# Optimization experiments

Measured on AMD Instinct MI355X. Metric: run time of the kernel, lower is better.

## Reference

```python
import jax, jax.numpy as jnp
import numpy as np

B, L, C, D, H, NB, K = 8, 1024, 4, 64, 8, 2, 16  # batch, seq, conds, dim, heads, blocks, rbf centers

def _ln(x, s, b):
    m = x.mean(-1, keepdims=True)
    v = x.var(-1, keepdims=True)
    return (x - m) / jnp.sqrt(v + 1e-6) * s + b

def setup_inputs() -> dict:
    key = jax.random.key(0)
    ks = jax.random.split(key, 24)
    rn = lambda i, shape, sc=0.02: jax.random.normal(ks[i], shape, jnp.float32) * sc
    inp = {}
    inp['z'] = jax.random.normal(ks[0], (B, L), jnp.float32)
    inp['conditionals'] = jax.random.normal(ks[1], (C,), jnp.float32)
    inp['s'] = jnp.sort(jax.random.uniform(ks[2], (L,), jnp.float32))
    inp['embed'] = rn(3, (L, 2 * D - (C + 1)))  # positional id embedding table
    # input MLP([4D, D]) with gelu
    inp['Win1'] = rn(4, (2 * D, 4 * D)); inp['bin1'] = jnp.zeros((4 * D,), jnp.float32)
    inp['Win2'] = rn(5, (4 * D, D));     inp['bin2'] = jnp.zeros((D,), jnp.float32)
    # per-block (leading dim NB) transformer params
    inp['ln1_s'] = jnp.ones((NB, D), jnp.float32); inp['ln1_b'] = jnp.zeros((NB, D), jnp.float32)
    inp['ln2_s'] = jnp.ones((NB, D), jnp.float32); inp['ln2_b'] = jnp.zeros((NB, D), jnp.float32)
    inp['Wq'] = rn(6, (NB, D, 2 * D)); inp['bq'] = jnp.zeros((NB, 2 * D), jnp.float32)
    inp['Wk'] = rn(7, (NB, D, 2 * D)); inp['bk'] = jnp.zeros((NB, 2 * D), jnp.float32)
    inp['Wv'] = rn(8, (NB, D, 2 * D)); inp['bv'] = jnp.zeros((NB, 2 * D), jnp.float32)
    inp['Wo'] = rn(9, (NB, 2 * D, D)); inp['bo'] = jnp.zeros((NB, D), jnp.float32)
    # RBF-network attention bias: features exp(-(d-c)^2/(2w^2)) -> linear to H heads
    inp['rbf_c'] = jnp.tile(jnp.linspace(-1.0, 1.0, K, dtype=jnp.float32)[None], (NB, 1))
    inp['rbf_logw'] = jnp.full((NB, K), -1.0, jnp.float32)
    inp['rbf_w'] = rn(10, (NB, K, H), 0.1); inp['rbf_b'] = jnp.zeros((NB, H), jnp.float32)
    # FFN MLP([4D, D])
    inp['W1'] = rn(11, (NB, D, 4 * D)); inp['b1'] = jnp.zeros((NB, 4 * D), jnp.float32)
    inp['W2'] = rn(12, (NB, 4 * D, D)); inp['b2'] = jnp.zeros((NB, D), jnp.float32)
    # head MLP([4D, D, 1])
    inp['Wh1'] = rn(13, (D, 4 * D)); inp['bh1'] = jnp.zeros((4 * D,), jnp.float32)
    inp['Wh2'] = rn(14, (4 * D, D)); inp['bh2'] = jnp.zeros((D,), jnp.float32)
    inp['Wh3'] = rn(15, (D, 1));     inp['bh3'] = jnp.zeros((1,), jnp.float32)
    return inp

def reference(z, conditionals, s, embed, Win1, bin1, Win2, bin2,
              ln1_s, ln1_b, ln2_s, ln2_b, Wq, bq, Wk, bk, Wv, bv, Wo, bo,
              rbf_c, rbf_logw, rbf_w, rbf_b, W1, b1, W2, b2,
              Wh1, bh1, Wh2, bh2, Wh3, bh3):
    Bn, Ln = z.shape
    Cn = conditionals.shape[0]
    Hn = rbf_w.shape[-1]
    dh = Wq.shape[-1] // Hn
    scale = 1.0 / jnp.sqrt(jnp.float32(dh))
    # cond_as_feats: [z, broadcast conditionals] -> (B, L, C+1); prepend ids embedding -> (B, L, 2D)
    feats = jnp.concatenate([
        jnp.broadcast_to(embed[None], (Bn,) + embed.shape),
        z[..., None],
        jnp.broadcast_to(conditionals[None, None, :], (Bn, Ln, Cn)),
    ], axis=-1)
    x = jax.nn.gelu(feats @ Win1 + bin1) @ Win2 + bin2  # (B, L, D)
    dist = s[:, None] - s[None, :]  # (L, L) pairwise query-key coordinate diff (same per batch)
    for i in range(Wq.shape[0]):
        h = _ln(x, ln1_s[i], ln1_b[i])
        q = (h @ Wq[i] + bq[i]).reshape(Bn, Ln, Hn, dh)
        k = (h @ Wk[i] + bk[i]).reshape(Bn, Ln, Hn, dh)
        v = (h @ Wv[i] + bv[i]).reshape(Bn, Ln, Hn, dh)
        scores = jnp.einsum('bqhd,bkhd->bhqk', q, k) * scale
        # RBF-network bias on pairwise distances, per head
        phi = jnp.exp(-(dist[..., None] - rbf_c[i]) ** 2 / (2.0 * jnp.exp(rbf_logw[i]) ** 2))  # (L, L, K)
        bias = jnp.einsum('qkf,fh->hqk', phi, rbf_w[i]) + rbf_b[i][:, None, None]  # (H, L, L)
        a = jax.nn.softmax(scores + bias[None], axis=-1)
        o = jnp.einsum('bhqk,bkhd->bqhd', a, v).reshape(Bn, Ln, Hn * dh)
        x = x + o @ Wo[i] + bo[i]
        h2 = _ln(x, ln2_s[i], ln2_b[i])
        x = x + jax.nn.gelu(h2 @ W1[i] + b1[i]) @ W2[i] + b2[i]
    hh = jax.nn.gelu(x @ Wh1 + bh1)
    hh = jax.nn.gelu(hh @ Wh2 + bh2)
    return hh @ Wh3 + bh3  # f_hat: (B, L, 1)
```

## Files before the change

kernel.cpp:

```cpp
#include <hip/hip_runtime.h>
#include <hip/hip_bf16.h>

#define BB   8
#define LL   1024
#define DD   64
#define D2   128
#define D4   256
#define HH   8
#define DH   16

typedef __attribute__((ext_vector_type(8))) short short8;
typedef __attribute__((ext_vector_type(4))) float floatx4;

#define OFF_WIN1   0
#define OFF_WIN2   65536
#define OFF_LAY0   98304
#define LAY_STRIDE 131072
#define OFF_WQ     0
#define OFF_WK     16384
#define OFF_WV     32768
#define OFF_WO     49152
#define OFF_W1     65536
#define OFF_W2     98304
#define OFF_WH1    360448
#define OFF_WH2    393216

__device__ __forceinline__ float gelu_tanh(float u) {
  float t = tanhf(0.7978845608028654f * (u + 0.044715f * u * u * u));
  return 0.5f * u * (1.0f + t);
}

__device__ __forceinline__ float wave_reduce_sum(float v) {
#pragma unroll
  for (int m = 32; m >= 1; m >>= 1) v += __shfl_xor(v, m, 64);
  return v;
}

__device__ __forceinline__ unsigned short f2bf(float x) {
  unsigned u = __float_as_uint(x);
  u += 0x7fffu + ((u >> 16) & 1u);
  return (unsigned short)(u >> 16);
}

__device__ __forceinline__ float bf2f(unsigned short x) {
  return __uint_as_float(((unsigned)x) << 16);
}

__device__ __forceinline__ void split_bf(float v, unsigned short& hi,
                                         unsigned short& lo) {
  hi = f2bf(v);
  lo = f2bf(v - bf2f(hi));
}

template <int K, int KP>
__device__ __forceinline__ floatx4 mfma_tile(
    const unsigned short* Ah, const unsigned short* Al,
    const unsigned short* __restrict__ Bh, const unsigned short* __restrict__ Bl,
    int lq, int quad, floatx4 C) {
#pragma unroll
  for (int kk = 0; kk < K; kk += 32) {
    short8 ah = *(const short8*)(Ah + lq * KP + kk + quad * 8);
    short8 al = *(const short8*)(Al + lq * KP + kk + quad * 8);
    short8 bh = *(const short8*)(Bh + lq * K + kk + quad * 8);
    short8 bl = *(const short8*)(Bl + lq * K + kk + quad * 8);
    C = __builtin_amdgcn_mfma_f32_16x16x32_bf16(ah, bh, C, 0, 0, 0);
    C = __builtin_amdgcn_mfma_f32_16x16x32_bf16(al, bh, C, 0, 0, 0);
    C = __builtin_amdgcn_mfma_f32_16x16x32_bf16(ah, bl, C, 0, 0, 0);
  }
  return C;
}

struct PrepArgs {
  const float* src[16];
  int Kd[16], Nd[16], dst[16], elems[16];
};

__global__ __launch_bounds__(256) void k_prep(PrepArgs a,
                                              unsigned short* __restrict__ arena) {
  int mid = blockIdx.y;
  int e = blockIdx.x * 256 + threadIdx.x;
  int KN = a.elems[mid];
  if (e >= KN) return;
  int K = a.Kd[mid], N = a.Nd[mid];
  int n = e / K, k = e - n * K;
  float wv = a.src[mid][k * N + n];
  unsigned short hi, lo;
  split_bf(wv, hi, lo);
  arena[a.dst[mid] + e] = hi;
  arena[a.dst[mid] + KN + e] = lo;
}

__global__ __launch_bounds__(256) void k_bias(
    const float* __restrict__ s, const float* __restrict__ rbf_c,
    const float* __restrict__ rbf_logw, const float* __restrict__ rbf_w,
    const float* __restrict__ rbf_b, unsigned short* __restrict__ biasT) {
  int lay = blockIdx.y;
  int id = blockIdx.x * 256 + threadIdx.x;
  int q = id >> 10, k = id & 1023;
  float dd = s[q] - s[k];
  float acc[8];
#pragma unroll
  for (int h = 0; h < 8; ++h) acc[h] = rbf_b[lay * 8 + h];
#pragma unroll 1
  for (int f = 0; f < 16; ++f) {
    float c = rbf_c[lay * 16 + f];
    float inv2w2 = 0.5f * __expf(-2.0f * rbf_logw[lay * 16 + f]);
    float e = dd - c;
    float ph = __expf(-e * e * inv2w2);
#pragma unroll
    for (int h = 0; h < 8; ++h)
      acc[h] = fmaf(ph, rbf_w[lay * 128 + f * 8 + h], acc[h]);
  }
  unsigned short* bT = biasT + (size_t)lay * 8 * 1024 * 1024;
#pragma unroll
  for (int h = 0; h < 8; ++h)
    bT[(size_t)(h * 1024 + q) * 1024 + k] = f2bf(acc[h]);
}

__device__ __forceinline__ void qkv_tail(
    const float* xl, unsigned short* Sh, unsigned short* Sl,
    const unsigned short* __restrict__ arena, int lay,
    const float* __restrict__ ln_s, const float* __restrict__ ln_b,
    const float* __restrict__ bq, const float* __restrict__ bk,
    const float* __restrict__ bv, unsigned short* __restrict__ qo,
    unsigned short* __restrict__ ko, unsigned short* __restrict__ voT,
    int tok0, int t) {
  int w = t >> 6, lane = t & 63;
  int lq = lane & 15, quad = lane >> 4;
  float ss = ln_s[lay * 64 + lane], sb = ln_b[lay * 64 + lane];
#pragma unroll
  for (int tk = 0; tk < 4; ++tk) {
    int tok = w * 4 + tk;
    float v = xl[tok * 64 + lane];
    float mean = wave_reduce_sum(v) * 0.015625f;
    float d = v - mean;
    float var = wave_reduce_sum(d * d) * 0.015625f;
    float hv = d * rsqrtf(var + 1e-6f) * ss + sb;
    unsigned short hi, lo;
    split_bf(hv, hi, lo);
    Sh[tok * 72 + lane] = hi;
    Sl[tok * 72 + lane] = lo;
  }
  __syncthreads();
  int b = tok0 >> 10, l0 = tok0 & 1023;
#pragma unroll 1
  for (int mat = 0; mat < 3; ++mat) {
    const unsigned short* Bh =
        arena + OFF_LAY0 + lay * LAY_STRIDE + mat * 16384;
    const unsigned short* Bl = Bh + 8192;
    const float* bias = (mat == 0 ? bq : mat == 1 ? bk : bv) + lay * 128;
#pragma unroll
    for (int j = 0; j < 2; ++j) {
      int tl = w + j * 4;
      int n = tl * 16 + lq;
      float bb = bias[n];
      floatx4 C = {bb, bb, bb, bb};
      C = mfma_tile<64, 72>(Sh, Sl, Bh + tl * 16 * 64, Bl + tl * 16 * 64,
                            lq, quad, C);
      if (mat < 2) {
        unsigned short* outp = (mat == 0 ? qo : ko);
        size_t basea = ((size_t)(b * 8 + tl) * 1024 + l0 + quad * 4) * 16 + lq;
#pragma unroll
        for (int r = 0; r < 4; ++r)
          outp[basea + (size_t)r * 16] = f2bf(C[r]);
      } else {
        size_t basev = ((size_t)(b * 8 + tl) * 16 + lq) * 1024 + l0 + quad * 4;
#pragma unroll
        for (int r = 0; r < 4; ++r)
          voT[basev + r] = f2bf(C[r]);
      }
    }
  }
}

__global__ __launch_bounds__(256) void k_in_qkv(
    const float* __restrict__ embed, const float* __restrict__ z,
    const float* __restrict__ cond, const unsigned short* __restrict__ arena,
    const float* __restrict__ bin1, const float* __restrict__ bin2,
    float* __restrict__ x, const float* __restrict__ ln1_s,
    const float* __restrict__ ln1_b, const float* __restrict__ bq,
    const float* __restrict__ bk, const float* __restrict__ bv,
    unsigned short* __restrict__ qo, unsigned short* __restrict__ ko,
    unsigned short* __restrict__ voT) {
  __shared__ __align__(16) unsigned short Ah[16 * 136], Al[16 * 136];
  __shared__ __align__(16) unsigned short Hh[16 * 264], Hl[16 * 264];
  __shared__ __align__(16) unsigned short Sh[16 * 72], Sl[16 * 72];
  __shared__ float xl[16 * 64];
  int t = threadIdx.x, w = t >> 6, lane = t & 63;
  int lq = lane & 15, quad = lane >> 4;
  int tok0 = blockIdx.x * 16;
  for (int idx = t; idx < 2048; idx += 256) {
    int tok = idx >> 7, dim = idx & 127;
    int bl = tok0 + tok, l = bl & (LL - 1);
    float v;
    if (dim < 123) v = embed[l * 123 + dim];
    else if (dim == 123) v = z[bl];
    else v = cond[dim - 124];
    unsigned short hi, lo;
    split_bf(v, hi, lo);
    Ah[tok * 136 + dim] = hi;
    Al[tok * 136 + dim] = lo;
  }
  __syncthreads();
  const unsigned short* B1h = arena + OFF_WIN1;
  const unsigned short* B1l = B1h + 32768;
#pragma unroll
  for (int j = 0; j < 4; ++j) {
    int tl = w * 4 + j, n = tl * 16 + lq;
    float bb = bin1[n];
    floatx4 C = {bb, bb, bb, bb};
    C = mfma_tile<128, 136>(Ah, Al, B1h + tl * 16 * 128, B1l + tl * 16 * 128,
                            lq, quad, C);
#pragma unroll
    for (int r = 0; r < 4; ++r) {
      float g = gelu_tanh(C[r]);
      unsigned short hi, lo;
      split_bf(g, hi, lo);
      Hh[(quad * 4 + r) * 264 + n] = hi;
      Hl[(quad * 4 + r) * 264 + n] = lo;
    }
  }
  __syncthreads();
  const unsigned short* B2h = arena + OFF_WIN2;
  const unsigned short* B2l = B2h + 16384;
  {
    int n = w * 16 + lq;
    float bb = bin2[n];
    floatx4 C = {bb, bb, bb, bb};
    C = mfma_tile<256, 264>(Hh, Hl, B2h + w * 16 * 256, B2l + w * 16 * 256,
                            lq, quad, C);
#pragma unroll
    for (int r = 0; r < 4; ++r) {
      int m = quad * 4 + r;
      x[(size_t)(tok0 + m) * 64 + n] = C[r];
      xl[m * 64 + n] = C[r];
    }
  }
  __syncthreads();
  qkv_tail(xl, Sh, Sl, arena, 0, ln1_s, ln1_b, bq, bk, bv,
           qo, ko, voT, tok0, t);
}

__global__ __launch_bounds__(256) void k_attn(
    const unsigned short* __restrict__ qg, const unsigned short* __restrict__ kg,
    const unsigned short* __restrict__ vgT, const unsigned short* __restrict__ biasT,
    float* __restrict__ og) {
  __shared__ __align__(16) unsigned short Kl[64 * 32];
  __shared__ __align__(16) unsigned short VT[16 * 72];
  __shared__ __align__(16) unsigned short Pl[4][16 * 72];
  __shared__ __align__(16) unsigned short Bch[64 * 72];
  int t = threadIdx.x, w = t >> 6, lane = t & 63;
  int lq = lane & 15, quad = lane >> 4;
  int bid = blockIdx.x;
  int b = bid >> 7, h = (bid >> 4) & 7, qblk = bid & 15;
  int q0w = qblk * 64 + w * 16;
  size_t bh = (size_t)(b * 8 + h) * 1024;
  size_t bh16 = (size_t)(b * 8 + h) * 16;

  ((uint4*)Kl)[t] = uint4{0, 0, 0, 0};

  short8 Qb = {};
  if (quad < 2)
    Qb = *(const short8*)(qg + (bh + q0w + lq) * 16 + quad * 8);

  float m = -1e30f, l = 0.0f;
  floatx4 O = {0.0f, 0.0f, 0.0f, 0.0f};

  int key = t >> 2, dp = (t & 3) * 4;
  int drow = t >> 4, vcol = (t & 15) * 4;
  int qrow = t >> 2, bcol = (t & 3) * 16;
  const unsigned short* kgp = kg + (bh + key) * 16 + dp;
  const unsigned short* vgp = vgT + (bh16 + drow) * 1024 + vcol;
  const unsigned short* bgp =
      biasT + ((size_t)(h * 1024 + qblk * 64 + qrow)) * 1024 + bcol;

  uint2 kpre = *(const uint2*)(kgp);
  uint2 vpre = *(const uint2*)(vgp);
  uint4 bpre0 = *(const uint4*)(bgp);
  uint4 bpre1 = *(const uint4*)(bgp + 8);

#pragma unroll 1
  for (int kc = 0; kc < 1024; kc += 64) {
    __syncthreads();
    *(uint2*)(Kl + key * 32 + dp) = kpre;
    *(uint2*)(VT + drow * 72 + vcol) = vpre;
    *(uint4*)(Bch + qrow * 72 + bcol) = bpre0;
    *(uint4*)(Bch + qrow * 72 + bcol + 8) = bpre1;
    __syncthreads();
    if (kc + 64 < 1024) {
      kpre = *(const uint2*)(kgp + (size_t)(kc + 64) * 16);
      vpre = *(const uint2*)(vgp + (kc + 64));
      bpre0 = *(const uint4*)(bgp + (kc + 64));
      bpre1 = *(const uint4*)(bgp + (kc + 64) + 8);
    }
    float s[16];
#pragma unroll
    for (int tile = 0; tile < 4; ++tile) {
      short8 A = *(const short8*)(Kl + (tile * 16 + lq) * 32 + quad * 8);
      floatx4 c = {0.0f, 0.0f, 0.0f, 0.0f};
      c = __builtin_amdgcn_mfma_f32_16x16x32_bf16(A, Qb, c, 0, 0, 0);
      ushort4 bb = *(const ushort4*)(Bch + (w * 16 + lq) * 72 +
                                     tile * 16 + quad * 4);
      s[tile * 4 + 0] = fmaf(c[0], 0.25f, bf2f(bb.x));
      s[tile * 4 + 1] = fmaf(c[1], 0.25f, bf2f(bb.y));
      s[tile * 4 + 2] = fmaf(c[2], 0.25f, bf2f(bb.z));
      s[tile * 4 + 3] = fmaf(c[3], 0.25f, bf2f(bb.w));
    }
    float cm = s[0];
#pragma unroll
    for (int i = 1; i < 16; ++i) cm = fmaxf(cm, s[i]);
    cm = fmaxf(cm, __shfl_xor(cm, 16, 64));
    cm = fmaxf(cm, __shfl_xor(cm, 32, 64));
    float mnew = fmaxf(m, cm);
    float alpha = __expf(m - mnew);
    float p[16], psum = 0.0f;
#pragma unroll
    for (int i = 0; i < 16; ++i) {
      p[i] = __expf(s[i] - mnew);
      psum += p[i];
    }
    psum += __shfl_xor(psum, 16, 64);
    psum += __shfl_xor(psum, 32, 64);
    l = l * alpha + psum;
    m = mnew;
    unsigned short* pw = &Pl[w][lq * 72];
#pragma unroll
    for (int tile = 0; tile < 4; ++tile) {
      uint2 pk;
      pk.x = (unsigned)f2bf(p[tile * 4 + 0]) | ((unsigned)f2bf(p[tile * 4 + 1]) << 16);
      pk.y = (unsigned)f2bf(p[tile * 4 + 2]) | ((unsigned)f2bf(p[tile * 4 + 3]) << 16);
      *(uint2*)(pw + tile * 16 + quad * 4) = pk;
    }
    asm volatile("s_waitcnt lgkmcnt(0)" ::: "memory");
#pragma unroll
    for (int r = 0; r < 4; ++r) {
      int idx = (quad * 4 + r) * 4;
      float ar = __uint_as_float(
          __builtin_amdgcn_ds_bpermute(idx, __float_as_uint(alpha)));
      O[r] *= ar;
    }
#pragma unroll
    for (int i = 0; i < 2; ++i) {
      short8 Pa = *(const short8*)(pw + i * 32 + quad * 8);
      short8 Vb = *(const short8*)(&VT[lq * 72 + i * 32 + quad * 8]);
      O = __builtin_amdgcn_mfma_f32_16x16x32_bf16(Pa, Vb, O, 0, 0, 0);
    }
  }
  float linv = 1.0f / l;
#pragma unroll
  for (int r = 0; r < 4; ++r) {
    int idx = (quad * 4 + r) * 4;
    float lr = __uint_as_float(
        __builtin_amdgcn_ds_bpermute(idx, __float_as_uint(linv)));
    og[((size_t)(b * 1024 + q0w + quad * 4 + r)) * 128 + h * 16 + lq] = O[r] * lr;
  }
}

__device__ __forceinline__ void pf_body(
    const float* __restrict__ ob, const unsigned short* __restrict__ arena,
    const float* __restrict__ bo, float* __restrict__ x,
    const float* __restrict__ ln_s, const float* __restrict__ ln_b,
    const float* __restrict__ b1, const float* __restrict__ b2, int lay,
    unsigned short* Ah, unsigned short* Al, unsigned short* Sh,
    unsigned short* Sl, unsigned short* Hh, unsigned short* Hl, float* xl,
    int tok0, int t, bool write_x) {
  int w = t >> 6, lane = t & 63;
  int lq = lane & 15, quad = lane >> 4;
  const unsigned short* labase = arena + OFF_LAY0 + lay * LAY_STRIDE;
  for (int idx = t * 4; idx < 2048; idx += 1024) {
    int row = idx >> 7, col = idx & 127;
    float4 v = *(const float4*)(ob + (size_t)(tok0 + row) * 128 + col);
    unsigned short h0, e0, h1, e1, h2, e2, h3, e3;
    split_bf(v.x, h0, e0); split_bf(v.y, h1, e1);
    split_bf(v.z, h2, e2); split_bf(v.w, h3, e3);
    unsigned* ph = (unsigned*)(Ah + row * 136 + col);
    ph[0] = (unsigned)h0 | ((unsigned)h1 << 16);
    ph[1] = (unsigned)h2 | ((unsigned)h3 << 16);
    unsigned* pl = (unsigned*)(Al + row * 136 + col);
    pl[0] = (unsigned)e0 | ((unsigned)e1 << 16);
    pl[1] = (unsigned)e2 | ((unsigned)e3 << 16);
  }
  __syncthreads();
  {
    const unsigned short* Bh = labase + OFF_WO;
    const unsigned short* Bl = Bh + 8192;
    int n = w * 16 + lq;
    float bb = bo[lay * 64 + n];
    floatx4 C = {bb, bb, bb, bb};
    C = mfma_tile<128, 136>(Ah, Al, Bh + w * 16 * 128, Bl + w * 16 * 128,
                            lq, quad, C);
#pragma unroll
    for (int r = 0; r < 4; ++r) {
      int m = quad * 4 + r;
      xl[m * 64 + n] = x[(size_t)(tok0 + m) * 64 + n] + C[r];
    }
  }
  __syncthreads();
  {
    float ss = ln_s[lay * 64 + lane], sb = ln_b[lay * 64 + lane];
#pragma unroll
    for (int tk = 0; tk < 4; ++tk) {
      int tok = w * 4 + tk;
      float v = xl[tok * 64 + lane];
      float mean = wave_reduce_sum(v) * 0.015625f;
      float d = v - mean;
      float var = wave_reduce_sum(d * d) * 0.015625f;
      float hv = d * rsqrtf(var + 1e-6f) * ss + sb;
      unsigned short hi, lo;
      split_bf(hv, hi, lo);
      Sh[tok * 72 + lane] = hi;
      Sl[tok * 72 + lane] = lo;
    }
  }
  __syncthreads();
  {
    const unsigned short* Bh = labase + OFF_W1;
    const unsigned short* Bl = Bh + 16384;
#pragma unroll
    for (int j = 0; j < 4; ++j) {
      int tl = w * 4 + j, n = tl * 16 + lq;
      float bb = b1[lay * 256 + n];
      floatx4 C = {bb, bb, bb, bb};
      C = mfma_tile<64, 72>(Sh, Sl, Bh + tl * 16 * 64, Bl + tl * 16 * 64,
                            lq, quad, C);
#pragma unroll
      for (int r = 0; r < 4; ++r) {
        float g = gelu_tanh(C[r]);
        unsigned short hi, lo;
        split_bf(g, hi, lo);
        Hh[(quad * 4 + r) * 264 + n] = hi;
        Hl[(quad * 4 + r) * 264 + n] = lo;
      }
    }
  }
  __syncthreads();
  {
    const unsigned short* Bh = labase + OFF_W2;
    const unsigned short* Bl = Bh + 16384;
    int n = w * 16 + lq;
    float bb = b2[lay * 64 + n];
    floatx4 C = {bb, bb, bb, bb};
    C = mfma_tile<256, 264>(Hh, Hl, Bh + w * 16 * 256, Bl + w * 16 * 256,
                            lq, quad, C);
#pragma unroll
    for (int r = 0; r < 4; ++r) {
      int m = quad * 4 + r;
      float xv = xl[m * 64 + n] + C[r];
      xl[m * 64 + n] = xv;
      if (write_x) x[(size_t)(tok0 + m) * 64 + n] = xv;
    }
  }
  __syncthreads();
}

__global__ __launch_bounds__(256) void k_pf_qkv(
    const float* __restrict__ ob, const unsigned short* __restrict__ arena,
    const float* __restrict__ bo, float* __restrict__ x,
    const float* __restrict__ ln2_s, const float* __restrict__ ln2_b,
    const float* __restrict__ b1, const float* __restrict__ b2, int lay,
    const float* __restrict__ ln1_s, const float* __restrict__ ln1_b,
    const float* __restrict__ bq, const float* __restrict__ bk,
    const float* __restrict__ bv, unsigned short* __restrict__ qo,
    unsigned short* __restrict__ ko, unsigned short* __restrict__ voT) {
  __shared__ __align__(16) unsigned short Ah[16 * 136], Al[16 * 136];
  __shared__ __align__(16) unsigned short Sh[16 * 72], Sl[16 * 72];
  __shared__ __align__(16) unsigned short Hh[16 * 264], Hl[16 * 264];
  __shared__ float xl[16 * 64];
  int t = threadIdx.x;
  int tok0 = blockIdx.x * 16;
  pf_body(ob, arena, bo, x, ln2_s, ln2_b, b1, b2, lay,
          Ah, Al, Sh, Sl, Hh, Hl, xl, tok0, t, true);
  qkv_tail(xl, Sh, Sl, arena, lay + 1, ln1_s, ln1_b, bq, bk, bv,
           qo, ko, voT, tok0, t);
}

__global__ __launch_bounds__(256) void k_pf_head(
    const float* __restrict__ ob, const unsigned short* __restrict__ arena,
    const float* __restrict__ bo, float* __restrict__ x,
    const float* __restrict__ ln2_s, const float* __restrict__ ln2_b,
    const float* __restrict__ b1, const float* __restrict__ b2, int lay,
    const float* __restrict__ bh1, const float* __restrict__ bh2,
    const float* __restrict__ Wh3, const float* __restrict__ bh3,
    float* __restrict__ out) {
  __shared__ __align__(16) unsigned short Ah[16 * 136], Al[16 * 136];
  __shared__ __align__(16) unsigned short Sh[16 * 72], Sl[16 * 72];
  __shared__ __align__(16) unsigned short Hh[16 * 264], Hl[16 * 264];
  __shared__ float xl[16 * 64];
  int t = threadIdx.x, w = t >> 6, lane = t & 63;
  int lq = lane & 15, quad = lane >> 4;
  int tok0 = blockIdx.x * 16;
  pf_body(ob, arena, bo, x, ln2_s, ln2_b, b1, b2, lay,
          Ah, Al, Sh, Sl, Hh, Hl, xl, tok0, t, false);
#pragma unroll
  for (int tk = 0; tk < 4; ++tk) {
    int tok = w * 4 + tk;
    unsigned short hi, lo;
    split_bf(xl[tok * 64 + lane], hi, lo);
    Sh[tok * 72 + lane] = hi;
    Sl[tok * 72 + lane] = lo;
  }
  __syncthreads();
  {
    const unsigned short* Bh = arena + OFF_WH1;
    const unsigned short* Bl = Bh + 16384;
#pragma unroll
    for (int j = 0; j < 4; ++j) {
      int tl = w * 4 + j, n = tl * 16 + lq;
      float bb = bh1[n];
      floatx4 C = {bb, bb, bb, bb};
      C = mfma_tile<64, 72>(Sh, Sl, Bh + tl * 16 * 64, Bl + tl * 16 * 64,
                            lq, quad, C);
#pragma unroll
      for (int r = 0; r < 4; ++r) {
        float g = gelu_tanh(C[r]);
        unsigned short hi, lo;
        split_bf(g, hi, lo);
        Hh[(quad * 4 + r) * 264 + n] = hi;
        Hl[(quad * 4 + r) * 264 + n] = lo;
      }
    }
  }
  __syncthreads();
  {
    const unsigned short* Bh = arena + OFF_WH2;
    const unsigned short* Bl = Bh + 16384;
    int n = w * 16 + lq;
    float bb = bh2[n];
    floatx4 C = {bb, bb, bb, bb};
    C = mfma_tile<256, 264>(Hh, Hl, Bh + w * 16 * 256, Bl + w * 16 * 256,
                            lq, quad, C);
    __syncthreads();
#pragma unroll
    for (int r = 0; r < 4; ++r)
      xl[(quad * 4 + r) * 64 + n] = gelu_tanh(C[r]);
  }
  __syncthreads();
  float wv3 = Wh3[lane];
#pragma unroll
  for (int tk = 0; tk < 4; ++tk) {
    int tok = w * 4 + tk;
    float v = xl[tok * 64 + lane] * wv3;
    float sum = wave_reduce_sum(v);
    if (lane == 0) out[tok0 + tok] = sum + bh3[0];
  }
}

extern "C" void kernel_launch(void* const* d_in, const int* in_sizes, int n_in,
                              void* d_out, int out_size, void* d_ws, size_t ws_size,
                              hipStream_t stream) {
  const float* z      = (const float*)d_in[0];
  const float* cond   = (const float*)d_in[1];
  const float* s      = (const float*)d_in[2];
  const float* embed  = (const float*)d_in[3];
  const float* Win1   = (const float*)d_in[4];
  const float* bin1   = (const float*)d_in[5];
  const float* Win2   = (const float*)d_in[6];
  const float* bin2   = (const float*)d_in[7];
  const float* ln1_s  = (const float*)d_in[8];
  const float* ln1_b  = (const float*)d_in[9];
  const float* ln2_s  = (const float*)d_in[10];
  const float* ln2_b  = (const float*)d_in[11];
  const float* Wq     = (const float*)d_in[12];
  const float* bq     = (const float*)d_in[13];
  const float* Wk     = (const float*)d_in[14];
  const float* bk     = (const float*)d_in[15];
  const float* Wv     = (const float*)d_in[16];
  const float* bv     = (const float*)d_in[17];
  const float* Wo     = (const float*)d_in[18];
  const float* bo     = (const float*)d_in[19];
  const float* rbf_c  = (const float*)d_in[20];
  const float* rbf_lw = (const float*)d_in[21];
  const float* rbf_w  = (const float*)d_in[22];
  const float* rbf_b  = (const float*)d_in[23];
  const float* W1     = (const float*)d_in[24];
  const float* b1     = (const float*)d_in[25];
  const float* W2     = (const float*)d_in[26];
  const float* b2     = (const float*)d_in[27];
  const float* Wh1    = (const float*)d_in[28];
  const float* bh1    = (const float*)d_in[29];
  const float* Wh2    = (const float*)d_in[30];
  const float* bh2    = (const float*)d_in[31];
  const float* Wh3    = (const float*)d_in[32];
  const float* bh3    = (const float*)d_in[33];

  char* base = (char*)d_ws;
  float*          x     = (float*)(base);
  unsigned short* qb    = (unsigned short*)(base + (2u << 20));
  unsigned short* kb    = (unsigned short*)(base + (4u << 20));
  unsigned short* vbT   = (unsigned short*)(base + (6u << 20));
  float*          ob    = (float*)(base + (8u << 20));
  unsigned short* biasT = (unsigned short*)(base + (12u << 20));
  unsigned short* arena = (unsigned short*)(base + (48u << 20));

  PrepArgs pa;
  auto set = [&](int i, const float* sp, int K, int N, int dst) {
    pa.src[i] = sp; pa.Kd[i] = K; pa.Nd[i] = N; pa.dst[i] = dst;
    pa.elems[i] = K * N;
  };
  set(0, Win1, 128, 256, OFF_WIN1);
  set(1, Win2, 256, 64, OFF_WIN2);
  for (int lay = 0; lay < 2; ++lay) {
    int lb = OFF_LAY0 + lay * LAY_STRIDE;
    set(2 + lay * 6, Wq + lay * 8192, 64, 128, lb + OFF_WQ);
    set(3 + lay * 6, Wk + lay * 8192, 64, 128, lb + OFF_WK);
    set(4 + lay * 6, Wv + lay * 8192, 64, 128, lb + OFF_WV);
    set(5 + lay * 6, Wo + lay * 8192, 128, 64, lb + OFF_WO);
    set(6 + lay * 6, W1 + lay * 16384, 64, 256, lb + OFF_W1);
    set(7 + lay * 6, W2 + lay * 16384, 256, 64, lb + OFF_W2);
  }
  set(14, Wh1, 64, 256, OFF_WH1);
  set(15, Wh2, 256, 64, OFF_WH2);

  k_prep<<<dim3(128, 16), 256, 0, stream>>>(pa, arena);
  k_bias<<<dim3(4096, 2), 256, 0, stream>>>(s, rbf_c, rbf_lw, rbf_w, rbf_b, biasT);
  k_in_qkv<<<512, 256, 0, stream>>>(embed, z, cond, arena, bin1, bin2, x,
                                    ln1_s, ln1_b, bq, bk, bv, qb, kb, vbT);
  k_attn<<<1024, 256, 0, stream>>>(qb, kb, vbT, biasT, ob);
  k_pf_qkv<<<512, 256, 0, stream>>>(ob, arena, bo, x, ln2_s, ln2_b, b1, b2, 0,
                                    ln1_s, ln1_b, bq, bk, bv, qb, kb, vbT);
  k_attn<<<1024, 256, 0, stream>>>(qb, kb, vbT,
                                   biasT + (size_t)8 * 1024 * 1024, ob);
  k_pf_head<<<512, 256, 0, stream>>>(ob, arena, bo, x, ln2_s, ln2_b, b1, b2, 1,
                                     bh1, bh2, Wh3, bh3, (float*)d_out);
}
```

Before: 275.4 us.

## Merge prep and bias kernels, use exp2 softmax, split MFMA accumulators

Merges the weight-split prep kernel and the RBF bias kernel into one launch, removing one kernel launch and the gap between them. The bias table and score scale are premultiplied by log2(e) so the softmax can use exp2f in place of __expf. The split-bf16 MFMA tile now keeps three independent accumulators so the three MFMAs per step no longer form one serial dependency chain. The exp2 rescaling changes bf16 rounding of the stored bias slightly.

```diff
diff --git a/kernel.cpp b/kernel.cpp
--- a/kernel.cpp
+++ b/kernel.cpp
@@ -11,6 +11,8 @@
 
 typedef __attribute__((ext_vector_type(8))) short short8;
 typedef __attribute__((ext_vector_type(4))) float floatx4;
+
+#define LOG2E 1.4426950408889634f
 
 #define OFF_WIN1   0
 #define OFF_WIN2   65536
@@ -57,16 +59,20 @@
     const unsigned short* Ah, const unsigned short* Al,
     const unsigned short* __restrict__ Bh, const unsigned short* __restrict__ Bl,
     int lq, int quad, floatx4 C) {
+  floatx4 C1 = {0.0f, 0.0f, 0.0f, 0.0f};
+  floatx4 C2 = {0.0f, 0.0f, 0.0f, 0.0f};
 #pragma unroll
   for (int kk = 0; kk < K; kk += 32) {
     short8 ah = *(const short8*)(Ah + lq * KP + kk + quad * 8);
     short8 al = *(const short8*)(Al + lq * KP + kk + quad * 8);
     short8 bh = *(const short8*)(Bh + lq * K + kk + quad * 8);
     short8 bl = *(const short8*)(Bl + lq * K + kk + quad * 8);
-    C = __builtin_amdgcn_mfma_f32_16x16x32_bf16(ah, bh, C, 0, 0, 0);
-    C = __builtin_amdgcn_mfma_f32_16x16x32_bf16(al, bh, C, 0, 0, 0);
-    C = __builtin_amdgcn_mfma_f32_16x16x32_bf16(ah, bl, C, 0, 0, 0);
-  }
+    C  = __builtin_amdgcn_mfma_f32_16x16x32_bf16(ah, bh, C, 0, 0, 0);
+    C1 = __builtin_amdgcn_mfma_f32_16x16x32_bf16(al, bh, C1, 0, 0, 0);
+    C2 = __builtin_amdgcn_mfma_f32_16x16x32_bf16(ah, bl, C2, 0, 0, 0);
+  }
+#pragma unroll
+  for (int r = 0; r < 4; ++r) C[r] += C1[r] + C2[r];
   return C;
 }
 
@@ -75,27 +81,29 @@
   int Kd[16], Nd[16], dst[16], elems[16];
 };
 
-__global__ __launch_bounds__(256) void k_prep(PrepArgs a,
-                                              unsigned short* __restrict__ arena) {
-  int mid = blockIdx.y;
-  int e = blockIdx.x * 256 + threadIdx.x;
-  int KN = a.elems[mid];
-  if (e >= KN) return;
-  int K = a.Kd[mid], N = a.Nd[mid];
-  int n = e / K, k = e - n * K;
-  float wv = a.src[mid][k * N + n];
-  unsigned short hi, lo;
-  split_bf(wv, hi, lo);
-  arena[a.dst[mid] + e] = hi;
-  arena[a.dst[mid] + KN + e] = lo;
-}
-
-__global__ __launch_bounds__(256) void k_bias(
+__global__ __launch_bounds__(256) void k_prep_bias(
+    PrepArgs a, unsigned short* __restrict__ arena,
     const float* __restrict__ s, const float* __restrict__ rbf_c,
     const float* __restrict__ rbf_logw, const float* __restrict__ rbf_w,
     const float* __restrict__ rbf_b, unsigned short* __restrict__ biasT) {
-  int lay = blockIdx.y;
-  int id = blockIdx.x * 256 + threadIdx.x;
+  int bid = blockIdx.x, t = threadIdx.x;
+  if (bid < 2048) {
+    int mid = bid >> 7;
+    int e = (bid & 127) * 256 + t;
+    int KN = a.elems[mid];
+    if (e >= KN) return;
+    int K = a.Kd[mid], N = a.Nd[mid];
+    int n = e / K, k = e - n * K;
+    float wv = a.src[mid][k * N + n];
+    unsigned short hi, lo;
+    split_bf(wv, hi, lo);
+    arena[a.dst[mid] + e] = hi;
+    arena[a.dst[mid] + KN + e] = lo;
+    return;
+  }
+  int rem = bid - 2048;
+  int lay = rem >> 12;
+  int id = (rem & 4095) * 256 + t;
   int q = id >> 10, k = id & 1023;
   float dd = s[q] - s[k];
   float acc[8];
@@ -114,7 +122,7 @@
   unsigned short* bT = biasT + (size_t)lay * 8 * 1024 * 1024;
 #pragma unroll
   for (int h = 0; h < 8; ++h)
-    bT[(size_t)(h * 1024 + q) * 1024 + k] = f2bf(acc[h]);
+    bT[(size_t)(h * 1024 + q) * 1024 + k] = f2bf(acc[h] * LOG2E);
 }
 
 __device__ __forceinline__ void qkv_tail(
@@ -301,10 +309,10 @@
       c = __builtin_amdgcn_mfma_f32_16x16x32_bf16(A, Qb, c, 0, 0, 0);
       ushort4 bb = *(const ushort4*)(Bch + (w * 16 + lq) * 72 +
                                      tile * 16 + quad * 4);
-      s[tile * 4 + 0] = fmaf(c[0], 0.25f, bf2f(bb.x));
-      s[tile * 4 + 1] = fmaf(c[1], 0.25f, bf2f(bb.y));
-      s[tile * 4 + 2] = fmaf(c[2], 0.25f, bf2f(bb.z));
-      s[tile * 4 + 3] = fmaf(c[3], 0.25f, bf2f(bb.w));
+      s[tile * 4 + 0] = fmaf(c[0], 0.25f * LOG2E, bf2f(bb.x));
+      s[tile * 4 + 1] = fmaf(c[1], 0.25f * LOG2E, bf2f(bb.y));
+      s[tile * 4 + 2] = fmaf(c[2], 0.25f * LOG2E, bf2f(bb.z));
+      s[tile * 4 + 3] = fmaf(c[3], 0.25f * LOG2E, bf2f(bb.w));
     }
     float cm = s[0];
 #pragma unroll
@@ -312,11 +320,11 @@
     cm = fmaxf(cm, __shfl_xor(cm, 16, 64));
     cm = fmaxf(cm, __shfl_xor(cm, 32, 64));
     float mnew = fmaxf(m, cm);
-    float alpha = __expf(m - mnew);
+    float alpha = exp2f(m - mnew);
     float p[16], psum = 0.0f;
 #pragma unroll
     for (int i = 0; i < 16; ++i) {
-      p[i] = __expf(s[i] - mnew);
+      p[i] = exp2f(s[i] - mnew);
       psum += p[i];
     }
     psum += __shfl_xor(psum, 16, 64);
@@ -611,8 +619,8 @@
   set(14, Wh1, 64, 256, OFF_WH1);
   set(15, Wh2, 256, 64, OFF_WH2);
 
-  k_prep<<<dim3(128, 16), 256, 0, stream>>>(pa, arena);
-  k_bias<<<dim3(4096, 2), 256, 0, stream>>>(s, rbf_c, rbf_lw, rbf_w, rbf_b, biasT);
+  k_prep_bias<<<2048 + 8192, 256, 0, stream>>>(pa, arena, s, rbf_c, rbf_lw,
+                                               rbf_w, rbf_b, biasT);
   k_in_qkv<<<512, 256, 0, stream>>>(embed, z, cond, arena, bin1, bin2, x,
                                     ln1_s, ln1_b, bq, bk, bv, qb, kb, vbT);
   k_attn<<<1024, 256, 0, stream>>>(qb, kb, vbT, biasT, ob);
```

New measurement: 285.4 us. +3.6%, slower.
